# Kernel optimization log

Hardware: AMD Instinct MI355X
Metric: run time of the kernel (lower is better)

The kernel has to match this reference:

```python
import jax, jax.numpy as jnp
import numpy as np
import math

DIM = 1024
B, S = 4, 2048

def setup_inputs() -> dict:
    key = jax.random.key(0)
    ks = jax.random.split(key, 4)
    scale = 1.0 / math.sqrt(DIM)
    X = jax.random.normal(ks[0], (B, S, DIM), dtype=jnp.float32)
    W_in = jax.random.normal(ks[1], (3 * DIM, DIM), dtype=jnp.float32) * scale
    b_in = jnp.zeros((3 * DIM,), dtype=jnp.float32)
    W_out = jax.random.normal(ks[2], (DIM, DIM), dtype=jnp.float32) * scale
    b_out = jnp.zeros((DIM,), dtype=jnp.float32)
    attention_mask = jnp.ones((B, 1, S), dtype=jnp.int32)
    return {"X": X, "attention_mask": attention_mask, "W_in": W_in,
            "b_in": b_in, "W_out": W_out, "b_out": b_out}

def reference(X, attention_mask, W_in, b_in, W_out, b_out):
    # in_proj: [B,S,3*DIM]
    qkv = jnp.einsum('bsd,ed->bse', X, W_in) + b_in
    Q, K, V = jnp.split(qkv, 3, axis=-1)
    # scores: [B,S,S]
    scores = jnp.einsum('bqd,bkd->bqk', Q, K)
    # masked_fill happens BEFORE the /sqrt(dim) scaling in the original
    scores = jnp.where(attention_mask == 0, jnp.float32(-1e20), scores)
    attn = jax.nn.softmax(scores / jnp.float32(math.sqrt(DIM)), axis=-1)
    # Dropout(0.1) treated as identity (eval-mode reference)
    out = jnp.einsum('bqk,bkd->bqd', attn, V)
    return jnp.einsum('bsd,od->bso', out, W_out) + b_out
```

## Files before the change

### kernel.cpp

```cpp
#include <hip/hip_runtime.h>
#include <stdint.h>

#define AS1 __attribute__((address_space(1)))
#define AS3 __attribute__((address_space(3)))

typedef __bf16 bf16x8 __attribute__((ext_vector_type(8)));
typedef float f32x16 __attribute__((ext_vector_type(16)));

__device__ __forceinline__ unsigned short f2bf(float f) {
  unsigned u = __float_as_uint(f);
  u += 0x7FFF + ((u >> 16) & 1);
  return (unsigned short)(u >> 16);
}
__device__ __forceinline__ float bf2f(unsigned short h) {
  return __uint_as_float(((unsigned)h) << 16);
}

__global__ __launch_bounds__(256) void cast_all_kernel(const float* __restrict__ X,
                                                       const float* __restrict__ Wi,
                                                       const float* __restrict__ Wo,
                                                       unsigned short* __restrict__ out) {
  const int c1 = 2097152;
  const int c2 = 786432;
  const int c3 = 262144;
  int i = blockIdx.x * 256 + threadIdx.x;
  if (i >= c1 + c2 + c3) return;
  const float* src;
  int j = i;
  if (i < c1) src = X;
  else if (i < c1 + c2) { src = Wi; j = i - c1; }
  else { src = Wo; j = i - c1 - c2; }
  float4 v = reinterpret_cast<const float4*>(src)[j];
  ushort4 o;
  o.x = f2bf(v.x); o.y = f2bf(v.y); o.z = f2bf(v.z); o.w = f2bf(v.w);
  reinterpret_cast<ushort4*>(out)[i] = o;
}

template<int MODE>
__global__ __launch_bounds__(256, 2) void gemm_bt128(
    const unsigned short* __restrict__ A, long lda, long strideA,
    const unsigned short* __restrict__ B, long ldb, long strideB,
    void* __restrict__ Cv, long ldc, long strideC,
    const float* __restrict__ bias, const int* __restrict__ mask,
    float* __restrict__ sums, unsigned short* __restrict__ vt, int K) {
  __shared__ unsigned short sA[128 * 64];
  __shared__ unsigned short sB[128 * 64];
  const int t = threadIdx.x;
  const int lane = t & 63;
  const int wave = t >> 6;

  const unsigned short* Ab = A + (size_t)blockIdx.z * strideA + (size_t)blockIdx.y * 128 * lda;
  const unsigned short* Bb = B + (size_t)blockIdx.z * strideB + (size_t)blockIdx.x * 128 * ldb;

  const int srow = t >> 3;
  const int schunk = (t & 7) ^ (srow & 7);
  const unsigned short* aptr = Ab + (size_t)srow * lda + schunk * 8;
  const unsigned short* bptr = Bb + (size_t)srow * ldb + schunk * 8;
  char* ldsA0 = (char*)&sA[0] + wave * 1024;
  char* ldsB0 = (char*)&sB[0] + wave * 1024;

  f32x16 acc[2][2];
#pragma unroll
  for (int i = 0; i < 2; i++)
#pragma unroll
    for (int j = 0; j < 2; j++)
#pragma unroll
      for (int r = 0; r < 16; r++) acc[i][j][r] = 0.f;

  const int wm = (wave >> 1) * 64;
  const int wn = (wave & 1) * 64;
  const int r31 = lane & 31;
  const int half = lane >> 5;
  const int swz = r31 & 7;

  int offA[2][4], offB[2][4];
#pragma unroll
  for (int i = 0; i < 2; i++)
#pragma unroll
    for (int s = 0; s < 4; s++) {
      offA[i][s] = (wm + i * 32 + r31) * 128 + (((2 * s + half) ^ swz) * 16);
      offB[i][s] = (wn + i * 32 + r31) * 128 + (((2 * s + half) ^ swz) * 16);
    }

  for (int k0 = 0; k0 < K; k0 += 64) {
    __syncthreads();
#pragma unroll
    for (int o = 0; o < 4; o++) {
      __builtin_amdgcn_global_load_lds((AS1 void*)(aptr + (size_t)o * 32 * lda + k0),
                                       (AS3 void*)(ldsA0 + o * 4096), 16, 0, 0);
      __builtin_amdgcn_global_load_lds((AS1 void*)(bptr + (size_t)o * 32 * ldb + k0),
                                       (AS3 void*)(ldsB0 + o * 4096), 16, 0, 0);
    }
    __syncthreads();
#pragma unroll
    for (int s = 0; s < 4; s++) {
      bf16x8 af[2], bfv[2];
#pragma unroll
      for (int i = 0; i < 2; i++) {
        af[i]  = *reinterpret_cast<const bf16x8*>((const char*)sA + offA[i][s]);
        bfv[i] = *reinterpret_cast<const bf16x8*>((const char*)sB + offB[i][s]);
      }
#pragma unroll
      for (int i = 0; i < 2; i++)
#pragma unroll
        for (int j = 0; j < 2; j++)
          acc[i][j] = __builtin_amdgcn_mfma_f32_32x32x16_bf16(af[i], bfv[j], acc[i][j], 0, 0, 0);
    }
  }

  const int* mrow = (MODE == 2) ? (mask + (size_t)blockIdx.z * 2048) : nullptr;
  const bool vblock = (MODE == 1) && (blockIdx.x >= 16);
  float rs[2][16];

#pragma unroll
  for (int i = 0; i < 2; i++) {
    int gmb = blockIdx.y * 128 + wm + i * 32;
    float inv_r[16];
    if (MODE == 3) {
#pragma unroll
      for (int r = 0; r < 16; r++) {
        int row = (r & 3) + 8 * (r >> 2) + 4 * half;
        inv_r[r] = 1.0f / sums[(size_t)blockIdx.z * 2048 + gmb + row];
      }
    }
    if (MODE == 2) {
#pragma unroll
      for (int r = 0; r < 16; r++) rs[i][r] = 0.f;
    }
#pragma unroll
    for (int j = 0; j < 2; j++) {
      int gn = blockIdx.x * 128 + wn + j * 32 + r31;
      float bv = (MODE == 0 || MODE == 1) ? bias[gn] : 0.0f;
      if (MODE == 1 && vblock) {
        int b = gmb >> 11;
        int sbase = gmb & 2047;
        int d = gn - 2048;
        unsigned short* vp = vt + (size_t)b * 1024 * 2048 + (size_t)d * 2048 + sbase + 4 * half;
#pragma unroll
        for (int qd = 0; qd < 4; qd++) {
          ushort4 o;
          o.x = f2bf(acc[i][j][4 * qd + 0] + bv);
          o.y = f2bf(acc[i][j][4 * qd + 1] + bv);
          o.z = f2bf(acc[i][j][4 * qd + 2] + bv);
          o.w = f2bf(acc[i][j][4 * qd + 3] + bv);
          *reinterpret_cast<ushort4*>(vp + 8 * qd) = o;
        }
      } else {
        bool msk = (MODE == 2) ? (mrow[gn] == 0) : false;
#pragma unroll
        for (int r = 0; r < 16; r++) {
          int row = (r & 3) + 8 * (r >> 2) + 4 * half;
          float val = acc[i][j][r] + bv;
          size_t off = (size_t)blockIdx.z * strideC + (size_t)(gmb + row) * ldc + gn;
          if (MODE == 2) {
            if (msk) val = -1e20f;
            val = __expf(val * 0.03125f);
            rs[i][r] += val;
            ((unsigned short*)Cv)[off] = f2bf(val);
          } else if (MODE == 3) {
            ((unsigned short*)Cv)[off] = f2bf(val * inv_r[r]);
          } else if (MODE == 1) {
            ((unsigned short*)Cv)[off] = f2bf(val);
          } else {
            ((float*)Cv)[off] = val;
          }
        }
      }
    }
  }

  if (MODE == 2) {
    float* srow = sums + (size_t)blockIdx.z * 2048;
#pragma unroll
    for (int i = 0; i < 2; i++) {
      int gmb = blockIdx.y * 128 + wm + i * 32;
#pragma unroll
      for (int r = 0; r < 16; r++) {
        float v = rs[i][r];
#pragma unroll
        for (int o = 16; o >= 1; o >>= 1) v += __shfl_xor(v, o, 64);
        if (r31 == 0) {
          int row = (r & 3) + 8 * (r >> 2) + 4 * half;
          atomicAdd(&srow[gmb + row], v);
        }
      }
    }
  }
}

extern "C" void kernel_launch(void* const* d_in, const int* in_sizes, int n_in,
                              void* d_out, int out_size, void* d_ws, size_t ws_size,
                              hipStream_t stream) {
  const float* X = (const float*)d_in[0];
  const int* mask = (const int*)d_in[1];
  const float* W_in = (const float*)d_in[2];
  const float* b_in = (const float*)d_in[3];
  const float* W_out = (const float*)d_in[4];
  const float* b_out = (const float*)d_in[5];
  float* out = (float*)d_out;

  const int S = 2048, D = 1024;
  char* w = (char*)d_ws;
  unsigned short* Xb  = (unsigned short*)w;
  unsigned short* Wib = (unsigned short*)(w + 16777216);
  unsigned short* Wob = (unsigned short*)(w + 16777216 + 6291456);
  unsigned short* QK  = (unsigned short*)(w + 25165824);
  unsigned short* P   = (unsigned short*)(w + 58720256);
  unsigned short* Vt  = (unsigned short*)(w + 92274688);
  float*          sums = (float*)(w + 109051904);
  unsigned short* Ob  = Xb;

  hipMemsetAsync(sums, 0, 8192 * sizeof(float), stream);

  cast_all_kernel<<<12288, 256, 0, stream>>>(X, W_in, W_out, Xb);

  gemm_bt128<1><<<dim3(24, 64, 1), 256, 0, stream>>>(
      Xb, D, 0, Wib, D, 0, QK, 2048, 0, b_in, nullptr, nullptr, Vt, D);
  gemm_bt128<2><<<dim3(16, 16, 4), 256, 0, stream>>>(
      QK, 2048, (long)S * 2048, QK + 1024, 2048, (long)S * 2048,
      P, S, (long)S * S, nullptr, mask, sums, nullptr, D);
  gemm_bt128<3><<<dim3(8, 16, 4), 256, 0, stream>>>(
      P, S, (long)S * S, Vt, S, (long)D * S,
      Ob, D, (long)S * D, nullptr, nullptr, sums, nullptr, S);
  gemm_bt128<0><<<dim3(8, 64, 1), 256, 0, stream>>>(
      Ob, D, 0, Wob, D, 0, out, D, 0, b_out, nullptr, nullptr, nullptr, D);
}
```

Before: 295.5 us.

## Rewrite GEMMs with 256-row tiles, LDS double buffering, and XCD-aware block remap

```diff
diff --git a/kernel.cpp b/kernel.cpp
--- a/kernel.cpp
+++ b/kernel.cpp
@@ -11,9 +11,6 @@
   unsigned u = __float_as_uint(f);
   u += 0x7FFF + ((u >> 16) & 1);
   return (unsigned short)(u >> 16);
-}
-__device__ __forceinline__ float bf2f(unsigned short h) {
-  return __uint_as_float(((unsigned)h) << 16);
 }
 
 __global__ __launch_bounds__(256) void cast_all_kernel(const float* __restrict__ X,
@@ -36,100 +33,165 @@
   reinterpret_cast<ushort4*>(out)[i] = o;
 }
 
-template<int MODE>
-__global__ __launch_bounds__(256, 2) void gemm_bt128(
+template<int MODE, int BNF>
+__global__ __launch_bounds__(512, 2) void gemm256(
     const unsigned short* __restrict__ A, long lda, long strideA,
     const unsigned short* __restrict__ B, long ldb, long strideB,
     void* __restrict__ Cv, long ldc, long strideC,
     const float* __restrict__ bias, const int* __restrict__ mask,
     float* __restrict__ sums, unsigned short* __restrict__ vt, int K) {
-  __shared__ unsigned short sA[128 * 64];
-  __shared__ unsigned short sB[128 * 64];
+  static_assert(BNF == 1 || BNF == 2, "BNF must be 1 or 2");
+  constexpr int BN = 128 * BNF;
+  constexpr int ABYTES = 256 * 128;
+  constexpr int BBYTES = BN * 128;
+  __shared__ unsigned short sA[2 * 256 * 64];
+  __shared__ unsigned short sB[2 * BN * 64];
+  char* sAc = (char*)sA;
+  char* sBc = (char*)sB;
+
   const int t = threadIdx.x;
   const int lane = t & 63;
   const int wave = t >> 6;
 
-  const unsigned short* Ab = A + (size_t)blockIdx.z * strideA + (size_t)blockIdx.y * 128 * lda;
-  const unsigned short* Bb = B + (size_t)blockIdx.z * strideB + (size_t)blockIdx.x * 128 * ldb;
+  const int nx = gridDim.x;
+  const int nwg = nx * gridDim.y;
+  int orig = blockIdx.y * nx + blockIdx.x;
+  int q = nwg >> 3, r8 = nwg & 7;
+  int xcd = orig & 7, idx = orig >> 3;
+  int wg = (xcd < r8 ? xcd * (q + 1) : r8 * (q + 1) + (xcd - r8) * q) + idx;
+  const int bx = wg % nx, by = wg / nx, bz = blockIdx.z;
+
+  const unsigned short* Ab = A + (size_t)bz * strideA + (size_t)by * 256 * lda;
+  const unsigned short* Bb = B + (size_t)bz * strideB + (size_t)bx * BN * ldb;
 
   const int srow = t >> 3;
-  const int schunk = (t & 7) ^ (srow & 7);
-  const unsigned short* aptr = Ab + (size_t)srow * lda + schunk * 8;
-  const unsigned short* bptr = Bb + (size_t)srow * ldb + schunk * 8;
-  char* ldsA0 = (char*)&sA[0] + wave * 1024;
-  char* ldsB0 = (char*)&sB[0] + wave * 1024;
-
-  f32x16 acc[2][2];
-#pragma unroll
-  for (int i = 0; i < 2; i++)
-#pragma unroll
-    for (int j = 0; j < 2; j++)
+  const int scol = ((t & 7) << 3) ^ ((srow & 7) << 3);
+  const unsigned short* aS = Ab + (size_t)srow * lda + scol;
+  const unsigned short* bS = Bb + (size_t)srow * ldb + scol;
+  const int ldsbase = (wave << 10);
+
+  const int NT = K >> 6;
+
+  f32x16 acc[4][BNF];
+#pragma unroll
+  for (int i = 0; i < 4; i++)
+#pragma unroll
+    for (int j = 0; j < BNF; j++)
 #pragma unroll
       for (int r = 0; r < 16; r++) acc[i][j][r] = 0.f;
 
-  const int wm = (wave >> 1) * 64;
-  const int wn = (wave & 1) * 64;
+  const int wm = (wave >> 2) << 7;
+  const int wn = (wave & 3) * (BNF << 5);
   const int r31 = lane & 31;
   const int half = lane >> 5;
-  const int swz = r31 & 7;
-
-  int offA[2][4], offB[2][4];
-#pragma unroll
-  for (int i = 0; i < 2; i++)
-#pragma unroll
-    for (int s = 0; s < 4; s++) {
-      offA[i][s] = (wm + i * 32 + r31) * 128 + (((2 * s + half) ^ swz) * 16);
-      offB[i][s] = (wn + i * 32 + r31) * 128 + (((2 * s + half) ^ swz) * 16);
-    }
-
-  for (int k0 = 0; k0 < K; k0 += 64) {
-    __syncthreads();
-#pragma unroll
-    for (int o = 0; o < 4; o++) {
-      __builtin_amdgcn_global_load_lds((AS1 void*)(aptr + (size_t)o * 32 * lda + k0),
-                                       (AS3 void*)(ldsA0 + o * 4096), 16, 0, 0);
-      __builtin_amdgcn_global_load_lds((AS1 void*)(bptr + (size_t)o * 32 * ldb + k0),
-                                       (AS3 void*)(ldsB0 + o * 4096), 16, 0, 0);
-    }
-    __syncthreads();
-#pragma unroll
-    for (int s = 0; s < 4; s++) {
-      bf16x8 af[2], bfv[2];
-#pragma unroll
-      for (int i = 0; i < 2; i++) {
-        af[i]  = *reinterpret_cast<const bf16x8*>((const char*)sA + offA[i][s]);
-        bfv[i] = *reinterpret_cast<const bf16x8*>((const char*)sB + offB[i][s]);
-      }
-#pragma unroll
-      for (int i = 0; i < 2; i++)
-#pragma unroll
-        for (int j = 0; j < 2; j++)
-          acc[i][j] = __builtin_amdgcn_mfma_f32_32x32x16_bf16(af[i], bfv[j], acc[i][j], 0, 0, 0);
-    }
+  int offK[4];
+#pragma unroll
+  for (int ks = 0; ks < 4; ks++)
+    offK[ks] = ((ks * 32 + half * 16) ^ ((r31 & 7) << 4));
+
+  auto stage = [&](int tk, int s) {
+    const unsigned short* ap = aS + tk * 64;
+#pragma unroll
+    for (int l = 0; l < 4; l++)
+      __builtin_amdgcn_global_load_lds((AS1 void*)(ap + (size_t)(l * 64) * lda),
+                                       (AS3 void*)(sAc + s * ABYTES + ldsbase + l * 8192),
+                                       16, 0, 0);
+    const unsigned short* bp = bS + tk * 64;
+#pragma unroll
+    for (int l = 0; l < 2 * BNF; l++)
+      __builtin_amdgcn_global_load_lds((AS1 void*)(bp + (size_t)(l * 64) * ldb),
+                                       (AS3 void*)(sBc + s * BBYTES + ldsbase + l * 8192),
+                                       16, 0, 0);
+  };
+
+  stage(0, 0);
+  stage(1, 1);
+  if constexpr (BNF == 2) {
+    asm volatile("s_waitcnt vmcnt(8)" ::: "memory");
+  } else {
+    asm volatile("s_waitcnt vmcnt(6)" ::: "memory");
   }
-
-  const int* mrow = (MODE == 2) ? (mask + (size_t)blockIdx.z * 2048) : nullptr;
-  const bool vblock = (MODE == 1) && (blockIdx.x >= 16);
-  float rs[2][16];
-
-#pragma unroll
-  for (int i = 0; i < 2; i++) {
-    int gmb = blockIdx.y * 128 + wm + i * 32;
+  __builtin_amdgcn_sched_barrier(0);
+  __builtin_amdgcn_s_barrier();
+
+  for (int tk = 0; tk < NT; ++tk) {
+    const int s = tk & 1;
+    const char* sa = sAc + s * ABYTES;
+    const char* sb = sBc + s * BBYTES;
+    bf16x8 bq[BNF][4];
+    bf16x8 aq[4];
+
+#pragma unroll
+    for (int ks = 0; ks < 4; ks++) {
+#pragma unroll
+      for (int j = 0; j < BNF; j++)
+        bq[j][ks] = *reinterpret_cast<const bf16x8*>(sb + (wn + 32 * j + r31) * 128 + offK[ks]);
+      aq[ks] = *reinterpret_cast<const bf16x8*>(sa + (wm + r31) * 128 + offK[ks]);
+    }
+    asm volatile("s_waitcnt lgkmcnt(0)" ::: "memory");
+    __builtin_amdgcn_sched_barrier(0);
+    __builtin_amdgcn_s_setprio(1);
+#pragma unroll
+    for (int ks = 0; ks < 4; ks++)
+#pragma unroll
+      for (int j = 0; j < BNF; j++)
+        acc[0][j] = __builtin_amdgcn_mfma_f32_32x32x16_bf16(aq[ks], bq[j][ks], acc[0][j], 0, 0, 0);
+    __builtin_amdgcn_s_setprio(0);
+
+#pragma unroll
+    for (int i = 1; i <= 2; i++) {
+#pragma unroll
+      for (int ks = 0; ks < 4; ks++)
+        aq[ks] = *reinterpret_cast<const bf16x8*>(sa + (wm + 32 * i + r31) * 128 + offK[ks]);
+      asm volatile("s_waitcnt lgkmcnt(0)" ::: "memory");
+      __builtin_amdgcn_sched_barrier(0);
+      __builtin_amdgcn_s_setprio(1);
+#pragma unroll
+      for (int ks = 0; ks < 4; ks++)
+#pragma unroll
+        for (int j = 0; j < BNF; j++)
+          acc[i][j] = __builtin_amdgcn_mfma_f32_32x32x16_bf16(aq[ks], bq[j][ks], acc[i][j], 0, 0, 0);
+      __builtin_amdgcn_s_setprio(0);
+    }
+
+#pragma unroll
+    for (int ks = 0; ks < 4; ks++)
+      aq[ks] = *reinterpret_cast<const bf16x8*>(sa + (wm + 96 + r31) * 128 + offK[ks]);
+    asm volatile("s_waitcnt vmcnt(0) lgkmcnt(0)" ::: "memory");
+    __builtin_amdgcn_sched_barrier(0);
+    __builtin_amdgcn_s_barrier();
+    if (tk + 2 < NT) stage(tk + 2, s);
+    __builtin_amdgcn_s_setprio(1);
+#pragma unroll
+    for (int ks = 0; ks < 4; ks++)
+#pragma unroll
+      for (int j = 0; j < BNF; j++)
+        acc[3][j] = __builtin_amdgcn_mfma_f32_32x32x16_bf16(aq[ks], bq[j][ks], acc[3][j], 0, 0, 0);
+    __builtin_amdgcn_s_setprio(0);
+  }
+
+  const int* mrow = (MODE == 2) ? (mask + (size_t)bz * 2048) : nullptr;
+  const bool vblock = (MODE == 1) && (bx >= 8);
+
+#pragma unroll
+  for (int i = 0; i < 4; i++) {
+    int gmb = by * 256 + wm + i * 32;
     float inv_r[16];
     if (MODE == 3) {
 #pragma unroll
       for (int r = 0; r < 16; r++) {
         int row = (r & 3) + 8 * (r >> 2) + 4 * half;
-        inv_r[r] = 1.0f / sums[(size_t)blockIdx.z * 2048 + gmb + row];
+        inv_r[r] = 1.0f / sums[(size_t)bz * 2048 + gmb + row];
       }
     }
+    float rs[16];
     if (MODE == 2) {
 #pragma unroll
-      for (int r = 0; r < 16; r++) rs[i][r] = 0.f;
-    }
-#pragma unroll
-    for (int j = 0; j < 2; j++) {
-      int gn = blockIdx.x * 128 + wn + j * 32 + r31;
+      for (int r = 0; r < 16; r++) rs[r] = 0.f;
+    }
+#pragma unroll
+    for (int j = 0; j < BNF; j++) {
+      int gn = bx * BN + wn + j * 32 + r31;
       float bv = (MODE == 0 || MODE == 1) ? bias[gn] : 0.0f;
       if (MODE == 1 && vblock) {
         int b = gmb >> 11;
@@ -151,11 +213,11 @@
         for (int r = 0; r < 16; r++) {
           int row = (r & 3) + 8 * (r >> 2) + 4 * half;
           float val = acc[i][j][r] + bv;
-          size_t off = (size_t)blockIdx.z * strideC + (size_t)(gmb + row) * ldc + gn;
+          size_t off = (size_t)bz * strideC + (size_t)(gmb + row) * ldc + gn;
           if (MODE == 2) {
             if (msk) val = -1e20f;
             val = __expf(val * 0.03125f);
-            rs[i][r] += val;
+            rs[r] += val;
             ((unsigned short*)Cv)[off] = f2bf(val);
           } else if (MODE == 3) {
             ((unsigned short*)Cv)[off] = f2bf(val * inv_r[r]);
@@ -167,21 +229,16 @@
         }
       }
     }
-  }
-
-  if (MODE == 2) {
-    float* srow = sums + (size_t)blockIdx.z * 2048;
-#pragma unroll
-    for (int i = 0; i < 2; i++) {
-      int gmb = blockIdx.y * 128 + wm + i * 32;
+    if (MODE == 2) {
+      float* srowp = sums + (size_t)bz * 2048;
 #pragma unroll
       for (int r = 0; r < 16; r++) {
-        float v = rs[i][r];
+        float v = rs[r];
 #pragma unroll
         for (int o = 16; o >= 1; o >>= 1) v += __shfl_xor(v, o, 64);
         if (r31 == 0) {
           int row = (r & 3) + 8 * (r >> 2) + 4 * half;
-          atomicAdd(&srow[gmb + row], v);
+          atomicAdd(&srowp[gmb + row], v);
         }
       }
     }
@@ -199,7 +256,7 @@
   const float* b_out = (const float*)d_in[5];
   float* out = (float*)d_out;
 
-  const int S = 2048, D = 1024;
+  const int S = 2048;
   char* w = (char*)d_ws;
   unsigned short* Xb  = (unsigned short*)w;
   unsigned short* Wib = (unsigned short*)(w + 16777216);
@@ -214,14 +271,14 @@
 
   cast_all_kernel<<<12288, 256, 0, stream>>>(X, W_in, W_out, Xb);
 
-  gemm_bt128<1><<<dim3(24, 64, 1), 256, 0, stream>>>(
-      Xb, D, 0, Wib, D, 0, QK, 2048, 0, b_in, nullptr, nullptr, Vt, D);
-  gemm_bt128<2><<<dim3(16, 16, 4), 256, 0, stream>>>(
+  gemm256<1, 2><<<dim3(12, 32, 1), 512, 0, stream>>>(
+      Xb, 1024, 0, Wib, 1024, 0, QK, 2048, 0, b_in, nullptr, nullptr, Vt, 1024);
+  gemm256<2, 2><<<dim3(8, 8, 4), 512, 0, stream>>>(
       QK, 2048, (long)S * 2048, QK + 1024, 2048, (long)S * 2048,
-      P, S, (long)S * S, nullptr, mask, sums, nullptr, D);
-  gemm_bt128<3><<<dim3(8, 16, 4), 256, 0, stream>>>(
-      P, S, (long)S * S, Vt, S, (long)D * S,
-      Ob, D, (long)S * D, nullptr, nullptr, sums, nullptr, S);
-  gemm_bt128<0><<<dim3(8, 64, 1), 256, 0, stream>>>(
-      Ob, D, 0, Wob, D, 0, out, D, 0, b_out, nullptr, nullptr, nullptr, D);
-}
+      P, 2048, (long)S * S, nullptr, mask, sums, nullptr, 1024);
+  gemm256<3, 1><<<dim3(8, 8, 4), 512, 0, stream>>>(
+      P, 2048, (long)S * S, Vt, 2048, (long)1024 * 2048,
+      Ob, 1024, (long)S * 1024, nullptr, nullptr, sums, nullptr, 2048);
+  gemm256<0, 1><<<dim3(8, 32, 1), 512, 0, stream>>>(
+      Ob, 1024, 0, Wob, 1024, 0, out, 1024, 0, b_out, nullptr, nullptr, nullptr, 1024);
+}
```

After: 317.7 us. +7.5%, slower.

## Add 256x256 multi-stage pipelined GEMM for QKV projection and scores

Applied to the files above, without the earlier changes.

```diff
diff --git a/kernel.cpp b/kernel.cpp
--- a/kernel.cpp
+++ b/kernel.cpp
@@ -11,9 +11,6 @@
   unsigned u = __float_as_uint(f);
   u += 0x7FFF + ((u >> 16) & 1);
   return (unsigned short)(u >> 16);
-}
-__device__ __forceinline__ float bf2f(unsigned short h) {
-  return __uint_as_float(((unsigned)h) << 16);
 }
 
 __global__ __launch_bounds__(256) void cast_all_kernel(const float* __restrict__ X,
@@ -37,6 +34,181 @@
 }
 
 template<int MODE>
+__global__ __launch_bounds__(512, 2) void gemmQ(
+    const unsigned short* __restrict__ A, long lda, long strideA,
+    const unsigned short* __restrict__ B, long ldb, long strideB,
+    void* __restrict__ Cv, long ldc, long strideC,
+    const float* __restrict__ bias, const int* __restrict__ mask,
+    float* __restrict__ sums, unsigned short* __restrict__ vt, int K) {
+  __shared__ unsigned short sAll[65536];
+  char* sBase = (char*)sAll;
+  const int t = threadIdx.x;
+  const int lane = t & 63;
+  const int wave = t >> 6;
+
+  const int nx = gridDim.x;
+  const int nwg = nx * gridDim.y;
+  int orig = blockIdx.y * nx + blockIdx.x;
+  int q = nwg >> 3, r8 = nwg & 7;
+  int xcd = orig & 7, idx = orig >> 3;
+  int wg = (xcd < r8 ? xcd * (q + 1) : r8 * (q + 1) + (xcd - r8) * q) + idx;
+  const int bx = wg % nx, by = wg / nx, bz = blockIdx.z;
+
+  const unsigned short* Ab = A + (size_t)bz * strideA + (size_t)by * 256 * lda;
+  const unsigned short* Bb = B + (size_t)bz * strideB + (size_t)bx * 256 * ldb;
+
+  const int srow = t >> 2;
+  const int scol = ((t & 3) ^ ((srow >> 1) & 3)) << 3;
+  const unsigned short* aS = Ab + (size_t)srow * lda + scol;
+  const unsigned short* bS = Bb + (size_t)srow * ldb + scol;
+
+  auto stage = [&](int tk, int s) {
+    char* base = sBase + s * 32768 + wave * 1024;
+    const unsigned short* ap = aS + tk * 32;
+    const unsigned short* bp = bS + tk * 32;
+#pragma unroll
+    for (int l = 0; l < 2; l++)
+      __builtin_amdgcn_global_load_lds((AS1 void*)(ap + (size_t)(l * 128) * lda),
+                                       (AS3 void*)(base + l * 8192), 16, 0, 0);
+#pragma unroll
+    for (int l = 0; l < 2; l++)
+      __builtin_amdgcn_global_load_lds((AS1 void*)(bp + (size_t)(l * 128) * ldb),
+                                       (AS3 void*)(base + 16384 + l * 8192), 16, 0, 0);
+  };
+
+  const int NT = K >> 5;
+
+  f32x16 acc[4][2];
+#pragma unroll
+  for (int i = 0; i < 4; i++)
+#pragma unroll
+    for (int j = 0; j < 2; j++)
+#pragma unroll
+      for (int r = 0; r < 16; r++) acc[i][j][r] = 0.f;
+
+  const int wm = (wave >> 2) << 7;
+  const int wn = (wave & 3) << 6;
+  const int r31 = lane & 31;
+  const int half = lane >> 5;
+  const int swz2 = (r31 >> 1) & 3;
+  int offC[2];
+#pragma unroll
+  for (int ks = 0; ks < 2; ks++)
+    offC[ks] = ((((ks << 1) + half) ^ swz2) << 4);
+  int rowA[4], rowB[2];
+#pragma unroll
+  for (int i = 0; i < 4; i++) rowA[i] = (wm + 32 * i + r31) << 6;
+#pragma unroll
+  for (int j = 0; j < 2; j++) rowB[j] = (wn + 32 * j + r31) << 6;
+
+  stage(0, 0);
+  stage(1, 1);
+  stage(2, 2);
+  asm volatile("s_waitcnt vmcnt(8)" ::: "memory");
+  __builtin_amdgcn_sched_barrier(0);
+  __builtin_amdgcn_s_barrier();
+  __builtin_amdgcn_sched_barrier(0);
+
+  for (int tk = 0; tk < NT; ++tk) {
+    const char* sa = sBase + (tk & 3) * 32768;
+    const char* sb = sa + 16384;
+    bf16x8 aq0[2], aq1[2], aq2[2], aq3[2], bq0[2], bq1[2];
+#pragma unroll
+    for (int ks = 0; ks < 2; ks++) {
+      bq0[ks] = *reinterpret_cast<const bf16x8*>(sb + rowB[0] + offC[ks]);
+      bq1[ks] = *reinterpret_cast<const bf16x8*>(sb + rowB[1] + offC[ks]);
+      aq0[ks] = *reinterpret_cast<const bf16x8*>(sa + rowA[0] + offC[ks]);
+      aq1[ks] = *reinterpret_cast<const bf16x8*>(sa + rowA[1] + offC[ks]);
+      aq2[ks] = *reinterpret_cast<const bf16x8*>(sa + rowA[2] + offC[ks]);
+      aq3[ks] = *reinterpret_cast<const bf16x8*>(sa + rowA[3] + offC[ks]);
+    }
+    __builtin_amdgcn_s_setprio(1);
+#pragma unroll
+    for (int ks = 0; ks < 2; ks++) {
+      acc[0][0] = __builtin_amdgcn_mfma_f32_32x32x16_bf16(aq0[ks], bq0[ks], acc[0][0], 0, 0, 0);
+      acc[0][1] = __builtin_amdgcn_mfma_f32_32x32x16_bf16(aq0[ks], bq1[ks], acc[0][1], 0, 0, 0);
+      acc[1][0] = __builtin_amdgcn_mfma_f32_32x32x16_bf16(aq1[ks], bq0[ks], acc[1][0], 0, 0, 0);
+      acc[1][1] = __builtin_amdgcn_mfma_f32_32x32x16_bf16(aq1[ks], bq1[ks], acc[1][1], 0, 0, 0);
+      acc[2][0] = __builtin_amdgcn_mfma_f32_32x32x16_bf16(aq2[ks], bq0[ks], acc[2][0], 0, 0, 0);
+      acc[2][1] = __builtin_amdgcn_mfma_f32_32x32x16_bf16(aq2[ks], bq1[ks], acc[2][1], 0, 0, 0);
+      acc[3][0] = __builtin_amdgcn_mfma_f32_32x32x16_bf16(aq3[ks], bq0[ks], acc[3][0], 0, 0, 0);
+      acc[3][1] = __builtin_amdgcn_mfma_f32_32x32x16_bf16(aq3[ks], bq1[ks], acc[3][1], 0, 0, 0);
+    }
+    __builtin_amdgcn_s_setprio(0);
+    if (tk == NT - 1) break;
+    __builtin_amdgcn_sched_barrier(0);
+    if (tk + 2 < NT) { asm volatile("s_waitcnt vmcnt(4)" ::: "memory"); }
+    else             { asm volatile("s_waitcnt vmcnt(0)" ::: "memory"); }
+    __builtin_amdgcn_sched_barrier(0);
+    __builtin_amdgcn_s_barrier();
+    __builtin_amdgcn_sched_barrier(0);
+    if (tk + 3 < NT) stage(tk + 3, (tk + 3) & 3);
+  }
+
+  const int* mrow = (MODE == 2) ? (mask + (size_t)bz * 2048) : nullptr;
+  const bool vblock = (MODE == 1) && (bx >= 8);
+
+#pragma unroll
+  for (int i = 0; i < 4; i++) {
+    int gmb = by * 256 + wm + i * 32;
+    float rs[16];
+    if (MODE == 2) {
+#pragma unroll
+      for (int r = 0; r < 16; r++) rs[r] = 0.f;
+    }
+#pragma unroll
+    for (int j = 0; j < 2; j++) {
+      int gn = bx * 256 + wn + j * 32 + r31;
+      float bv = (MODE == 1) ? bias[gn] : 0.0f;
+      if (MODE == 1 && vblock) {
+        int b = gmb >> 11;
+        int sbase = gmb & 2047;
+        int d = gn - 2048;
+        unsigned short* vp = vt + (size_t)b * 1024 * 2048 + (size_t)d * 2048 + sbase + 4 * half;
+#pragma unroll
+        for (int qd = 0; qd < 4; qd++) {
+          ushort4 o;
+          o.x = f2bf(acc[i][j][4 * qd + 0] + bv);
+          o.y = f2bf(acc[i][j][4 * qd + 1] + bv);
+          o.z = f2bf(acc[i][j][4 * qd + 2] + bv);
+          o.w = f2bf(acc[i][j][4 * qd + 3] + bv);
+          *reinterpret_cast<ushort4*>(vp + 8 * qd) = o;
+        }
+      } else {
+        bool msk = (MODE == 2) ? (mrow[gn] == 0) : false;
+#pragma unroll
+        for (int r = 0; r < 16; r++) {
+          int row = (r & 3) + 8 * (r >> 2) + 4 * half;
+          float val = acc[i][j][r] + bv;
+          size_t off = (size_t)bz * strideC + (size_t)(gmb + row) * ldc + gn;
+          if (MODE == 2) {
+            if (msk) val = -1e20f;
+            val = __expf(val * 0.03125f);
+            rs[r] += val;
+            ((unsigned short*)Cv)[off] = f2bf(val);
+          } else {
+            ((unsigned short*)Cv)[off] = f2bf(val);
+          }
+        }
+      }
+    }
+    if (MODE == 2) {
+      float* srowp = sums + (size_t)bz * 2048;
+#pragma unroll
+      for (int r = 0; r < 16; r++) {
+        float v = rs[r];
+#pragma unroll
+        for (int o = 16; o >= 1; o >>= 1) v += __shfl_xor(v, o, 64);
+        if (r31 == 0) {
+          int row = (r & 3) + 8 * (r >> 2) + 4 * half;
+          atomicAdd(&srowp[gmb + row], v);
+        }
+      }
+    }
+  }
+}
+
+template<int MODE>
 __global__ __launch_bounds__(256, 2) void gemm_bt128(
     const unsigned short* __restrict__ A, long lda, long strideA,
     const unsigned short* __restrict__ B, long ldb, long strideB,
@@ -108,10 +280,6 @@
     }
   }
 
-  const int* mrow = (MODE == 2) ? (mask + (size_t)blockIdx.z * 2048) : nullptr;
-  const bool vblock = (MODE == 1) && (blockIdx.x >= 16);
-  float rs[2][16];
-
 #pragma unroll
   for (int i = 0; i < 2; i++) {
     int gmb = blockIdx.y * 128 + wm + i * 32;
@@ -123,65 +291,19 @@
         inv_r[r] = 1.0f / sums[(size_t)blockIdx.z * 2048 + gmb + row];
       }
     }
-    if (MODE == 2) {
-#pragma unroll
-      for (int r = 0; r < 16; r++) rs[i][r] = 0.f;
-    }
 #pragma unroll
     for (int j = 0; j < 2; j++) {
       int gn = blockIdx.x * 128 + wn + j * 32 + r31;
-      float bv = (MODE == 0 || MODE == 1) ? bias[gn] : 0.0f;
-      if (MODE == 1 && vblock) {
-        int b = gmb >> 11;
-        int sbase = gmb & 2047;
-        int d = gn - 2048;
-        unsigned short* vp = vt + (size_t)b * 1024 * 2048 + (size_t)d * 2048 + sbase + 4 * half;
-#pragma unroll
-        for (int qd = 0; qd < 4; qd++) {
-          ushort4 o;
-          o.x = f2bf(acc[i][j][4 * qd + 0] + bv);
-          o.y = f2bf(acc[i][j][4 * qd + 1] + bv);
-          o.z = f2bf(acc[i][j][4 * qd + 2] + bv);
-          o.w = f2bf(acc[i][j][4 * qd + 3] + bv);
-          *reinterpret_cast<ushort4*>(vp + 8 * qd) = o;
-        }
-      } else {
-        bool msk = (MODE == 2) ? (mrow[gn] == 0) : false;
-#pragma unroll
-        for (int r = 0; r < 16; r++) {
-          int row = (r & 3) + 8 * (r >> 2) + 4 * half;
-          float val = acc[i][j][r] + bv;
-          size_t off = (size_t)blockIdx.z * strideC + (size_t)(gmb + row) * ldc + gn;
-          if (MODE == 2) {
-            if (msk) val = -1e20f;
-            val = __expf(val * 0.03125f);
-            rs[i][r] += val;
-            ((unsigned short*)Cv)[off] = f2bf(val);
-          } else if (MODE == 3) {
-            ((unsigned short*)Cv)[off] = f2bf(val * inv_r[r]);
-          } else if (MODE == 1) {
-            ((unsigned short*)Cv)[off] = f2bf(val);
-          } else {
-            ((float*)Cv)[off] = val;
-          }
-        }
-      }
-    }
-  }
-
-  if (MODE == 2) {
-    float* srow = sums + (size_t)blockIdx.z * 2048;
-#pragma unroll
-    for (int i = 0; i < 2; i++) {
-      int gmb = blockIdx.y * 128 + wm + i * 32;
+      float bv = (MODE == 0) ? bias[gn] : 0.0f;
 #pragma unroll
       for (int r = 0; r < 16; r++) {
-        float v = rs[i][r];
-#pragma unroll
-        for (int o = 16; o >= 1; o >>= 1) v += __shfl_xor(v, o, 64);
-        if (r31 == 0) {
-          int row = (r & 3) + 8 * (r >> 2) + 4 * half;
-          atomicAdd(&srow[gmb + row], v);
+        int row = (r & 3) + 8 * (r >> 2) + 4 * half;
+        float val = acc[i][j][r] + bv;
+        size_t off = (size_t)blockIdx.z * strideC + (size_t)(gmb + row) * ldc + gn;
+        if (MODE == 3) {
+          ((unsigned short*)Cv)[off] = f2bf(val * inv_r[r]);
+        } else {
+          ((float*)Cv)[off] = val;
         }
       }
     }
@@ -214,9 +336,9 @@
 
   cast_all_kernel<<<12288, 256, 0, stream>>>(X, W_in, W_out, Xb);
 
-  gemm_bt128<1><<<dim3(24, 64, 1), 256, 0, stream>>>(
+  gemmQ<1><<<dim3(12, 32, 1), 512, 0, stream>>>(
       Xb, D, 0, Wib, D, 0, QK, 2048, 0, b_in, nullptr, nullptr, Vt, D);
-  gemm_bt128<2><<<dim3(16, 16, 4), 256, 0, stream>>>(
+  gemmQ<2><<<dim3(8, 8, 4), 512, 0, stream>>>(
       QK, 2048, (long)S * 2048, QK + 1024, 2048, (long)S * 2048,
       P, S, (long)S * S, nullptr, mask, sums, nullptr, D);
   gemm_bt128<3><<<dim3(8, 16, 4), 256, 0, stream>>>(
```

New measurement: 315.0 us. +6.6%, slower.
